# Kernel optimization log

Measured on AMD Instinct MI355X. Metric: run time of the kernel, lower is better.

## Reference

```python
import jax, jax.numpy as jnp
import numpy as np

N = 50000
E = 1600000
D_IN = 64
D_H = 64
D_EMB = 64
D_DEC = 128
B = 4096


def setup_inputs() -> dict:
    key = jax.random.key(0)
    ks = jax.random.split(key, 16)
    def lin(k, fan_in, fan_out):
        return jax.random.normal(k, (fan_in, fan_out), jnp.float32) / np.sqrt(fan_in)
    inp = {
        "x": jax.random.normal(ks[0], (N, D_IN), jnp.float32),
        "edge_index": jax.random.randint(ks[1], (2, E), 0, N),
        "drug_index": jax.random.randint(ks[2], (B, 2), 1, N),
        "bn_gamma": jnp.ones((D_IN,), jnp.float32),
        "bn_beta": jnp.zeros((D_IN,), jnp.float32),
        "Wu1": lin(ks[3], D_IN, D_H), "Wd1": lin(ks[4], D_IN, D_H), "Wb1": lin(ks[5], D_IN, D_H),
        "Wu2": lin(ks[6], 3 * D_H, D_H), "Wd2": lin(ks[7], 3 * D_H, D_H), "Wb2": lin(ks[8], 3 * D_H, D_H),
        "Wu3": lin(ks[9], 3 * D_H, D_EMB), "Wd3": lin(ks[10], 3 * D_H, D_EMB), "Wb3": lin(ks[11], 3 * D_H, D_EMB),
        "P1": jax.random.normal(ks[12], (3 * D_EMB, D_DEC), jnp.float32),
        "P2": jax.random.normal(ks[13], (D_DEC, D_DEC), jnp.float32),
    }
    return inp


def _batchnorm(x, gamma, beta, eps=1e-5):
    mu = jnp.mean(x, axis=0)
    var = jnp.var(x, axis=0)  # biased, matches torch BN training normalization
    return gamma * (x - mu) / jnp.sqrt(var + eps) + beta


def _bgnn_conv(x, row, col, Wu, Wd, Wb, n_nodes):
    # up direction: messages flow row -> col (source_to_target)
    up = x @ Wu
    dn = x @ Wd
    bi = x @ Wb
    ones = jnp.ones(row.shape[0], x.dtype)
    deg_up = jax.ops.segment_sum(ones, col, num_segments=n_nodes)  # in-degree at col
    x_up = jax.ops.segment_sum(up[row] / deg_up[col][:, None], col, num_segments=n_nodes)
    # down direction: flipped edge_index -> messages flow col -> row
    deg_dn = jax.ops.segment_sum(ones, row, num_segments=n_nodes)
    x_dn = jax.ops.segment_sum(dn[col] / deg_dn[row][:, None], row, num_segments=n_nodes)
    c = jnp.concatenate([x_up, x_dn, bi], axis=-1)
    nrm = jnp.linalg.norm(c, axis=-1, keepdims=True)
    return c / jnp.maximum(nrm, 1e-12)


def _leaky(t):
    return jnp.where(t >= 0, t, 0.1 * t)


def reference(x, edge_index, drug_index, bn_gamma, bn_beta,
              Wu1, Wd1, Wb1, Wu2, Wd2, Wb2, Wu3, Wd3, Wb3, P1, P2):
    row, col = edge_index[0], edge_index[1]
    h = _batchnorm(x, bn_gamma, bn_beta)
    h = _leaky(_bgnn_conv(h, row, col, Wu1, Wd1, Wb1, N))
    h = _leaky(_bgnn_conv(h, row, col, Wu2, Wd2, Wb2, N))
    h = _leaky(_bgnn_conv(h, row, col, Wu3, Wd3, Wb3, N))
    di = jnp.reshape(drug_index, (-1, 2))
    a = h[di[:, 0] - 1]  # [B, 3*D_EMB]
    b = h[di[:, 1] - 1]
    M = P1 @ P2 @ P1.T  # [3*D_EMB, 3*D_EMB]
    ypred = jnp.einsum('bd,de,be->b', a, M, b)[:, None]
    return ypred
```

## Files before the change

kernel.cpp:

```cpp
#include <hip/hip_runtime.h>

#define PN 50000
#define PE 1600000
#define PB 4096
#define NP 8
#define PSZ 6250
#define NSW 4
#define SWSZ 12500
#define SCAP 210000
#define NSL 4
#define GBLK 2048
#define NPER 7

typedef __attribute__((ext_vector_type(8))) short bf16x8;
typedef __attribute__((ext_vector_type(4))) float f32x4;

__device__ inline float b2f(ushort u) {
    union { unsigned int i; float f; } x; x.i = ((unsigned int)u) << 16; return x.f;
}
__device__ inline ushort f2b(float f) {
    union { float f; unsigned int i; } x; x.f = f;
    unsigned int r = (x.i + 0x7FFFu + ((x.i >> 16) & 1u)) >> 16;
    return (ushort)r;
}

static constexpr size_t L4N = 4 * (size_t)PN;
static constexpr size_t IDXCAP3 = PE + 3 * L4N + 1024;
static constexpr size_t OFF_BN     = 0;
static constexpr size_t OFF_GCUR   = 256;
static constexpr size_t OFF_TMPM   = 272;
static constexpr size_t OFF_M      = OFF_TMPM + 192 * 128;
static constexpr size_t OFF_WOFFU  = OFF_M + 192 * 192;
static constexpr size_t OFF_WOFFD  = OFF_WOFFU + L4N + 4;
static constexpr size_t OFF_WDEGU  = OFF_WOFFD + L4N + 4;
static constexpr size_t OFF_WDEGD  = OFF_WDEGU + L4N;
static constexpr size_t OFF_PHISTU = OFF_WDEGD + L4N;
static constexpr size_t OFF_PHISTD = OFF_PHISTU + NSL * L4N;
static constexpr size_t OFF_IDXU   = OFF_PHISTD + NSL * L4N;
static constexpr size_t OFF_IDXD   = OFF_IDXU + (IDXCAP3 + 1) / 2;
static constexpr size_t OFF_STGU   = OFF_IDXD + (IDXCAP3 + 1) / 2;
static constexpr size_t OFF_STGD   = OFF_STGU + NP * (size_t)SCAP;
static constexpr size_t OFF_WB16   = OFF_STGD + NP * (size_t)SCAP;
static constexpr size_t OFF_HB     = OFF_WB16 + 43008;
static constexpr size_t OFF_PROJ   = OFF_HB + (size_t)PN * 96;

__global__ __launch_bounds__(256) void bn_stats_kernel(const float* __restrict__ x,
                                                       float* __restrict__ sums, int N) {
    __shared__ float ls[256], ls2[256];
    int col = threadIdx.x & 63;
    int rstart = blockIdx.x * 4 + (threadIdx.x >> 6);
    float s = 0.f, s2 = 0.f;
    for (int r = rstart; r < N; r += gridDim.x * 4) {
        float v = x[(size_t)r * 64 + col];
        s += v; s2 += v * v;
    }
    ls[threadIdx.x] = s; ls2[threadIdx.x] = s2;
    __syncthreads();
    if (threadIdx.x < 64) {
        s  = ls[threadIdx.x]  + ls[threadIdx.x + 64]  + ls[threadIdx.x + 128]  + ls[threadIdx.x + 192];
        s2 = ls2[threadIdx.x] + ls2[threadIdx.x + 64] + ls2[threadIdx.x + 128] + ls2[threadIdx.x + 192];
        atomicAdd(&sums[col], s);
        atomicAdd(&sums[64 + col], s2);
    }
}

__global__ __launch_bounds__(64) void bn_finalize_kernel(const float* __restrict__ gamma,
                                                         const float* __restrict__ beta,
                                                         float* __restrict__ bn, int N) {
    int c = threadIdx.x;
    float mean = bn[c] / (float)N;
    float var = bn[64 + c] / (float)N - mean * mean;
    float sc = gamma[c] * rsqrtf(var + 1e-5f);
    bn[128 + c] = sc;
    bn[192 + c] = beta[c] - mean * sc;
}

__global__ __launch_bounds__(256) void bin_kernel(const int* __restrict__ ei,
                                                  int* __restrict__ gcur,
                                                  uint* __restrict__ stgu,
                                                  uint* __restrict__ stgd, int E) {
    __shared__ uint sbuf[16][1024];
    __shared__ int scnt[16], sbase[16];
    const int tid = threadIdx.x;
    for (int base = blockIdx.x * 1024; base < E; base += gridDim.x * 1024) {
        if (tid < 16) scnt[tid] = 0;
        __syncthreads();
#pragma unroll
        for (int j = 0; j < 4; ++j) {
            int e = base + j * 256 + tid;
            if (e < E) {
                int r = __builtin_nontemporal_load(&ei[e]);
                int c = __builtin_nontemporal_load(&ei[E + e]);
                int pu = c / PSZ;
                int slot = atomicAdd(&scnt[pu], 1);
                sbuf[pu][slot] = ((uint)c << 16) | (uint)r;
                int pd = r / PSZ;
                int slot2 = atomicAdd(&scnt[8 + pd], 1);
                sbuf[8 + pd][slot2] = ((uint)r << 16) | (uint)c;
            }
        }
        __syncthreads();
        if (tid < 16) sbase[tid] = atomicAdd(&gcur[tid], scnt[tid]);
        __syncthreads();
#pragma unroll 1
        for (int k = 0; k < 16; ++k) {
            int cnt = scnt[k];
            int gb = sbase[k];
            uint* dst = (k < 8) ? (stgu + (size_t)k * SCAP) : (stgd + (size_t)(k - 8) * SCAP);
            for (int i = tid; i < cnt; i += 256) {
                int gi = gb + i;
                if (gi < SCAP) dst[gi] = sbuf[k][i];
            }
        }
        __syncthreads();
    }
}

__global__ __launch_bounds__(256) void hist_kernel(const uint* __restrict__ stgu,
                                                   const uint* __restrict__ stgd,
                                                   const int* __restrict__ gcur,
                                                   int* __restrict__ phistu,
                                                   int* __restrict__ phistd) {
    __shared__ int hist[PSZ * NSW];
    const int p = blockIdx.x & 7;
    const int dir = (blockIdx.x >> 3) & 1;
    const int s = blockIdx.x >> 4;
    const int tid = threadIdx.x;
    const int lo = p * PSZ;
    for (int i = tid; i < PSZ * NSW; i += 256) hist[i] = 0;
    __syncthreads();
    const int cnt = min(gcur[dir * 8 + p], SCAP);
    const uint* stg = (dir ? stgd : stgu) + (size_t)p * SCAP;
    const int per = (cnt + NSL - 1) / NSL;
    const int s0 = s * per, s1 = min(cnt, s0 + per);
    for (int i = s0 + tid; i < s1; i += 256) {
        uint u = stg[i];
        int ld = (int)(u >> 16) - lo;
        int w = (int)(u & 0xFFFFu) / SWSZ;
        atomicAdd(&hist[ld * NSW + w], 1);
    }
    __syncthreads();
    int* ph = (dir ? phistd : phistu) + (size_t)s * L4N + (size_t)lo * NSW;
    for (int i = tid; i < PSZ * NSW; i += 256) ph[i] = hist[i];
}

__global__ __launch_bounds__(1024) void scan_kernel(const int* __restrict__ phA,
                                                    const int* __restrict__ phB,
                                                    int* __restrict__ offA,
                                                    int* __restrict__ offB,
                                                    int* __restrict__ degA,
                                                    int* __restrict__ degB, int len) {
    const int* ph = blockIdx.x ? phB : phA;
    int* off = blockIdx.x ? offB : offA;
    int* dego = blockIdx.x ? degB : degA;
    __shared__ int wsum[17];
    int tid = threadIdx.x, lane = tid & 63, wid = tid >> 6;
    int run = 0;
    for (int base = 0; base < len; base += 4096) {
        int i4 = base + tid * 4;
        int4 v = make_int4(0, 0, 0, 0);
        if (i4 < len) {
#pragma unroll
            for (int sl = 0; sl < NSL; ++sl) {
                int4 t = *(const int4*)&ph[(size_t)sl * len + i4];
                v.x += t.x; v.y += t.y; v.z += t.z; v.w += t.w;
            }
            *(int4*)&dego[i4] = v;
        }
        v.x = (v.x + 3) & ~3; v.y = (v.y + 3) & ~3;
        v.z = (v.z + 3) & ~3; v.w = (v.w + 3) & ~3;
        int lsum = v.x + v.y + v.z + v.w;
        int inc = lsum;
#pragma unroll
        for (int d = 1; d < 64; d <<= 1) {
            int t = __shfl_up(inc, d);
            if (lane >= d) inc += t;
        }
        if (lane == 63) wsum[wid] = inc;
        __syncthreads();
        if (tid == 0) {
            int r2 = 0;
#pragma unroll
            for (int i = 0; i < 16; ++i) { int t = wsum[i]; wsum[i] = r2; r2 += t; }
            wsum[16] = r2;
        }
        __syncthreads();
        if (i4 < len) {
            int pre = run + wsum[wid] + inc - lsum;
            int4 o;
            o.x = pre; o.y = pre + v.x; o.z = o.y + v.y; o.w = o.z + v.z;
            *(int4*)&off[i4] = o;
        }
        run += wsum[16];
        __syncthreads();
    }
    if (tid == 0) off[len] = run;
}

__global__ __launch_bounds__(256) void scatter_kernel(const uint* __restrict__ stgu,
                                                      const uint* __restrict__ stgd,
                                                      const int* __restrict__ gcur,
                                                      const int* __restrict__ phistu,
                                                      const int* __restrict__ phistd,
                                                      const int* __restrict__ woffu,
                                                      const int* __restrict__ woffd,
                                                      ushort* __restrict__ idxu,
                                                      ushort* __restrict__ idxd) {
    __shared__ int cur[PSZ * NSW];
    const int p = blockIdx.x & 7;
    const int dir = (blockIdx.x >> 3) & 1;
    const int s = blockIdx.x >> 4;
    const int tid = threadIdx.x;
    const int lo = p * PSZ;
    const int* off = (dir ? woffd : woffu);
    const int* phist = (dir ? phistd : phistu);
    const size_t gb = (size_t)lo * NSW;
    for (int i = tid; i < PSZ * NSW; i += 256) {
        int c = off[gb + i];
        for (int t = 0; t < s; ++t) c += phist[(size_t)t * L4N + gb + i];
        cur[i] = c;
    }
    __syncthreads();
    const int cnt = min(gcur[dir * 8 + p], SCAP);
    const uint* stg = (dir ? stgd : stgu) + (size_t)p * SCAP;
    ushort* idx = (dir ? idxd : idxu);
    const int per = (cnt + NSL - 1) / NSL;
    const int s0 = s * per, s1 = min(cnt, s0 + per);
    for (int i = s0 + tid; i < s1; i += 256) {
        uint u = stg[i];
        int src = (int)(u & 0xFFFFu);
        int li = ((int)(u >> 16) - lo) * NSW + src / SWSZ;
        int pos = atomicAdd(&cur[li], 1);
        idx[pos] = (ushort)src;
    }
}

template<int K>
__global__ __launch_bounds__(256) void wconv_kernel(const float* __restrict__ Wu,
                                                    const float* __restrict__ Wd,
                                                    const float* __restrict__ Wb,
                                                    ushort* __restrict__ out) {
    int idx = blockIdx.x * 256 + threadIdx.x;
    if (idx >= 192 * K) return;
    int c = idx / K, k = idx - c * K;
    const float* W = (c < 64) ? Wu : (c < 128 ? Wd : Wb);
    out[idx] = f2b(W[k * 64 + (c & 63)]);
}

template<int K, bool BN>
__global__ __launch_bounds__(256) void gemm_kernel(const ushort* __restrict__ hb,
                                                   const float* __restrict__ x,
                                                   const float* __restrict__ bn,
                                                   const ushort* __restrict__ wb,
                                                   ushort* __restrict__ proj, int nrows) {
    constexpr int KP = K + 8;
    __shared__ ushort wlds[192 * KP];
    const int tid = threadIdx.x;
    constexpr int KB8 = K / 8;
    for (int idx = tid; idx < 192 * KB8; idx += 256) {
        int col = idx / KB8, kb = idx - col * KB8;
        *(bf16x8*)&wlds[col * KP + kb * 8] = *(const bf16x8*)&wb[(size_t)col * K + kb * 8];
    }
    __syncthreads();
    const int lane = tid & 63, wid = tid >> 6;
    const int kgrp = (lane >> 4) * 8;
    const int rbase = blockIdx.x * 128 + wid * 32;
    int ar[2] = { min(rbase + (lane & 15), nrows - 1),
                  min(rbase + 16 + (lane & 15), nrows - 1) };
    f32x4 acc[2][12];
#pragma unroll
    for (int rt = 0; rt < 2; ++rt)
#pragma unroll
        for (int ct = 0; ct < 12; ++ct) acc[rt][ct] = (f32x4)0.0f;

#pragma unroll
    for (int k0 = 0; k0 < K; k0 += 32) {
        bf16x8 af[2];
        if (BN) {
#pragma unroll
            for (int rt = 0; rt < 2; ++rt)
#pragma unroll
                for (int j = 0; j < 8; ++j) {
                    int c = k0 + kgrp + j;
                    float v = x[(size_t)ar[rt] * 64 + c] * bn[128 + c] + bn[192 + c];
                    af[rt][j] = (short)f2b(v);
                }
        } else {
#pragma unroll
            for (int rt = 0; rt < 2; ++rt)
                af[rt] = *(const bf16x8*)&hb[(size_t)ar[rt] * 192 + k0 + kgrp];
        }
#pragma unroll
        for (int ct = 0; ct < 12; ++ct) {
            bf16x8 bfr = *(const bf16x8*)&wlds[(ct * 16 + (lane & 15)) * KP + k0 + kgrp];
            acc[0][ct] = __builtin_amdgcn_mfma_f32_16x16x32_bf16(af[0], bfr, acc[0][ct], 0, 0, 0);
            acc[1][ct] = __builtin_amdgcn_mfma_f32_16x16x32_bf16(af[1], bfr, acc[1][ct], 0, 0, 0);
        }
    }
    const int orow0 = blockIdx.x * 128 + wid * 32 + (lane >> 4) * 4;
#pragma unroll
    for (int rt = 0; rt < 2; ++rt)
#pragma unroll
        for (int ct = 0; ct < 12; ++ct) {
            int ocol = ct * 16 + (lane & 15);
#pragma unroll
            for (int j = 0; j < 4; ++j) {
                int orow = orow0 + rt * 16 + j;
                if (orow < nrows) proj[(size_t)orow * 192 + ocol] = f2b(acc[rt][ct][j]);
            }
        }
}

__global__ __launch_bounds__(256) void gather_kernel(const ushort* __restrict__ proj,
                                                     const int* __restrict__ woffu,
                                                     const int* __restrict__ wdegu,
                                                     const int* __restrict__ woffd,
                                                     const int* __restrict__ wdegd,
                                                     const ushort* __restrict__ idxu,
                                                     const ushort* __restrict__ idxd,
                                                     ushort* __restrict__ hb, int N) {
    const int gw = blockIdx.x * 4 + (threadIdx.x >> 6);
    const int nwaves = gridDim.x * 4;
    const int lane = threadIdx.x & 63;
    const int half = lane >> 5;
    const int sl = lane & 31;
    const int* __restrict__ woff = half ? woffd : woffu;
    const int* __restrict__ wdeg = half ? wdegd : wdegu;
    const ushort* __restrict__ idx = half ? idxd : idxu;
    const uint* __restrict__ rowb = (const uint*)proj + half * 32 + sl;

    float a0[NPER], a1[NPER];
    int dtot[NPER];
#pragma unroll
    for (int j = 0; j < NPER; ++j) { a0[j] = 0.f; a1[j] = 0.f; dtot[j] = 0; }

    for (int w = 0; w < NSW; ++w) {
#pragma unroll
        for (int j = 0; j < NPER; ++j) {
            int n = gw + j * nwaves;
            if (n < N) {
                int key = n * NSW + w;
                int s = woff[key];
                int cnt = wdeg[key];
                dtot[j] += cnt;
                const ushort* p = idx + s;
                for (int i = 0; i < cnt; i += 4) {
                    ushort4 U = *(const ushort4*)(p + i);
                    int v1 = (i + 1 < cnt), v2 = (i + 2 < cnt), v3 = (i + 3 < cnt);
                    int s0 = (int)U.x;
                    int s1 = v1 ? (int)U.y : 0;
                    int s2 = v2 ? (int)U.z : 0;
                    int s3 = v3 ? (int)U.w : 0;
                    uint w0 = rowb[(size_t)s0 * 96];
                    uint w1 = rowb[(size_t)s1 * 96];
                    uint w2 = rowb[(size_t)s2 * 96];
                    uint w3 = rowb[(size_t)s3 * 96];
                    if (!v1) w1 = 0; if (!v2) w2 = 0; if (!v3) w3 = 0;
                    a0[j] += __uint_as_float(w0 << 16) + __uint_as_float(w1 << 16)
                           + __uint_as_float(w2 << 16) + __uint_as_float(w3 << 16);
                    a1[j] += __uint_as_float(w0 & 0xFFFF0000u) + __uint_as_float(w1 & 0xFFFF0000u)
                           + __uint_as_float(w2 & 0xFFFF0000u) + __uint_as_float(w3 & 0xFFFF0000u);
                }
            }
        }
        __syncthreads();
    }

    uint* hb32 = (uint*)hb;
#pragma unroll
    for (int j = 0; j < NPER; ++j) {
        int n = gw + j * nwaves;
        if (n >= N) continue;
        float sc = 1.0f / (float)max(dtot[j], 1);
        float A0 = a0[j] * sc, A1 = a1[j] * sc;
        uint bw = (half == 0) ? ((const uint*)proj)[(size_t)n * 96 + 64 + sl] : 0u;
        float b0 = __uint_as_float(bw << 16);
        float b1 = __uint_as_float(bw & 0xFFFF0000u);
        float ss = A0 * A0 + A1 * A1 + b0 * b0 + b1 * b1;
#pragma unroll
        for (int off = 32; off; off >>= 1) ss += __shfl_xor(ss, off);
        float r = 1.0f / fmaxf(sqrtf(ss), 1e-12f);
        A0 *= r; A1 *= r; b0 *= r; b1 *= r;
        A0 = A0 >= 0.f ? A0 : 0.1f * A0;
        A1 = A1 >= 0.f ? A1 : 0.1f * A1;
        hb32[(size_t)n * 96 + half * 32 + sl] = (uint)f2b(A0) | ((uint)f2b(A1) << 16);
        if (half == 0) {
            b0 = b0 >= 0.f ? b0 : 0.1f * b0;
            b1 = b1 >= 0.f ? b1 : 0.1f * b1;
            hb32[(size_t)n * 96 + 64 + sl] = (uint)f2b(b0) | ((uint)f2b(b1) << 16);
        }
    }
}

__global__ __launch_bounds__(128) void m1_kernel(const float* __restrict__ P1,
                                                 const float* __restrict__ P2,
                                                 float* __restrict__ tmpM) {
    int i = blockIdx.x, c = threadIdx.x;
    float s = 0.f;
    for (int k = 0; k < 128; ++k) s += P1[i * 128 + k] * P2[k * 128 + c];
    tmpM[i * 128 + c] = s;
}

__global__ __launch_bounds__(192) void m2_kernel(const float* __restrict__ tmpM,
                                                 const float* __restrict__ P1,
                                                 float* __restrict__ M) {
    __shared__ float trow[128];
    int i = blockIdx.x, j = threadIdx.x;
    if (j < 128) trow[j] = tmpM[i * 128 + j];
    __syncthreads();
    float s = 0.f;
    for (int k = 0; k < 128; ++k) s += trow[k] * P1[j * 128 + k];
    M[i * 192 + j] = s;
}

__global__ __launch_bounds__(192) void decode_kernel(const ushort* __restrict__ hb,
                                                     const int* __restrict__ di,
                                                     const float* __restrict__ M,
                                                     float* __restrict__ out) {
    __shared__ alignas(16) float bvs[8][192];
    __shared__ float red[3][8];
    int pb = blockIdx.x * 8;
    int i = threadIdx.x;
#pragma unroll
    for (int p = 0; p < 8; ++p) {
        int nb = di[(pb + p) * 2 + 1] - 1;
        bvs[p][i] = b2f(hb[(size_t)nb * 192 + i]);
    }
    __syncthreads();
    float t[8] = {};
    const float4* M4 = (const float4*)(M + (size_t)i * 192);
    for (int j4 = 0; j4 < 48; ++j4) {
        float4 m = M4[j4];
#pragma unroll
        for (int p = 0; p < 8; ++p) {
            float4 b = *(const float4*)&bvs[p][j4 * 4];
            t[p] += m.x * b.x + m.y * b.y + m.z * b.z + m.w * b.w;
        }
    }
    int wid = i >> 6, lane = i & 63;
#pragma unroll
    for (int p = 0; p < 8; ++p) {
        int na = di[(pb + p) * 2] - 1;
        float v = b2f(hb[(size_t)na * 192 + i]) * t[p];
#pragma unroll
        for (int off = 32; off; off >>= 1) v += __shfl_xor(v, off);
        if (lane == 0) red[wid][p] = v;
    }
    __syncthreads();
    if (i < 8) out[pb + i] = red[0][i] + red[1][i] + red[2][i];
}

extern "C" void kernel_launch(void* const* d_in, const int* in_sizes, int n_in,
                              void* d_out, int out_size, void* d_ws, size_t ws_size,
                              hipStream_t stream) {
    const float* x     = (const float*)d_in[0];
    const int*   ei    = (const int*)d_in[1];
    const int*   di    = (const int*)d_in[2];
    const float* gamma = (const float*)d_in[3];
    const float* beta  = (const float*)d_in[4];
    const float* Wu[3] = {(const float*)d_in[5], (const float*)d_in[8],  (const float*)d_in[11]};
    const float* Wd[3] = {(const float*)d_in[6], (const float*)d_in[9],  (const float*)d_in[12]};
    const float* Wb[3] = {(const float*)d_in[7], (const float*)d_in[10], (const float*)d_in[13]};
    const float* P1    = (const float*)d_in[14];
    const float* P2    = (const float*)d_in[15];
    float* out = (float*)d_out;
    float* ws  = (float*)d_ws;

    float* bn    = ws + OFF_BN;
    int* gcur  = (int*)(ws + OFF_GCUR);
    float* tmpM  = ws + OFF_TMPM;
    float* M     = ws + OFF_M;
    int* woffu = (int*)(ws + OFF_WOFFU);
    int* woffd = (int*)(ws + OFF_WOFFD);
    int* wdegu = (int*)(ws + OFF_WDEGU);
    int* wdegd = (int*)(ws + OFF_WDEGD);
    int* phistu = (int*)(ws + OFF_PHISTU);
    int* phistd = (int*)(ws + OFF_PHISTD);
    ushort* idxu = (ushort*)(ws + OFF_IDXU);
    ushort* idxd = (ushort*)(ws + OFF_IDXD);
    uint* stgu = (uint*)(ws + OFF_STGU);
    uint* stgd = (uint*)(ws + OFF_STGD);
    ushort* wb16 = (ushort*)(ws + OFF_WB16);
    ushort* hb   = (ushort*)(ws + OFF_HB);
    ushort* proj = (ushort*)(ws + OFF_PROJ);
    ushort* wbl[3] = {wb16, wb16 + 12288, wb16 + 49152};

    hipMemsetAsync(ws, 0, 272 * sizeof(float), stream);

    bn_stats_kernel<<<200, 256, 0, stream>>>(x, bn, PN);
    bn_finalize_kernel<<<1, 64, 0, stream>>>(gamma, beta, bn, PN);

    bin_kernel<<<512, 256, 0, stream>>>(ei, gcur, stgu, stgd, PE);
    hist_kernel<<<16 * NSL, 256, 0, stream>>>(stgu, stgd, gcur, phistu, phistd);
    scan_kernel<<<2, 1024, 0, stream>>>(phistu, phistd, woffu, woffd, wdegu, wdegd, (int)L4N);
    scatter_kernel<<<16 * NSL, 256, 0, stream>>>(stgu, stgd, gcur, phistu, phistd,
                                                 woffu, woffd, idxu, idxd);

    wconv_kernel<64><<<(192 * 64 + 255) / 256, 256, 0, stream>>>(Wu[0], Wd[0], Wb[0], wbl[0]);
    wconv_kernel<192><<<(192 * 192 + 255) / 256, 256, 0, stream>>>(Wu[1], Wd[1], Wb[1], wbl[1]);
    wconv_kernel<192><<<(192 * 192 + 255) / 256, 256, 0, stream>>>(Wu[2], Wd[2], Wb[2], wbl[2]);

    const int ngb = (PN + 127) / 128;
    gemm_kernel<64, true><<<ngb, 256, 0, stream>>>(hb, x, bn, wbl[0], proj, PN);
    gather_kernel<<<GBLK, 256, 0, stream>>>(proj, woffu, wdegu, woffd, wdegd, idxu, idxd, hb, PN);
    gemm_kernel<192, false><<<ngb, 256, 0, stream>>>(hb, x, bn, wbl[1], proj, PN);
    gather_kernel<<<GBLK, 256, 0, stream>>>(proj, woffu, wdegu, woffd, wdegd, idxu, idxd, hb, PN);
    gemm_kernel<192, false><<<ngb, 256, 0, stream>>>(hb, x, bn, wbl[2], proj, PN);
    gather_kernel<<<GBLK, 256, 0, stream>>>(proj, woffu, wdegu, woffd, wdegd, idxu, idxd, hb, PN);

    m1_kernel<<<192, 128, 0, stream>>>(P1, P2, tmpM);
    m2_kernel<<<192, 192, 0, stream>>>(tmpM, P1, M);
    decode_kernel<<<PB / 8, 192, 0, stream>>>(hb, di, M, out);
}
```

Measured before the change: 752.3 us.

## Split hist/scatter by destination sub-range instead of edge slices

Hist and scatter blocks now each own a 625-node destination sub-range and scan the whole partition's staged edges, filtering by range. Previously blocks split the edge list into slices and wrote per-slice histograms that had to be summed in the scan and prefix-summed in scatter. This removes the per-slice histogram buffers, the extra scan reads and the scatter prefix loop. It also shrinks LDS per block and raises block count from 64 to 160. The cost is that each staged edge is read 10 times instead of once.

```diff
diff --git a/kernel.cpp b/kernel.cpp
--- a/kernel.cpp
+++ b/kernel.cpp
@@ -8,7 +8,8 @@
 #define NSW 4
 #define SWSZ 12500
 #define SCAP 210000
-#define NSL 4
+#define SP 10
+#define SPSZ 625
 #define GBLK 2048
 #define NPER 7
 
@@ -34,9 +35,7 @@
 static constexpr size_t OFF_WOFFD  = OFF_WOFFU + L4N + 4;
 static constexpr size_t OFF_WDEGU  = OFF_WOFFD + L4N + 4;
 static constexpr size_t OFF_WDEGD  = OFF_WDEGU + L4N;
-static constexpr size_t OFF_PHISTU = OFF_WDEGD + L4N;
-static constexpr size_t OFF_PHISTD = OFF_PHISTU + NSL * L4N;
-static constexpr size_t OFF_IDXU   = OFF_PHISTD + NSL * L4N;
+static constexpr size_t OFF_IDXU   = OFF_WDEGD + L4N;
 static constexpr size_t OFF_IDXD   = OFF_IDXU + (IDXCAP3 + 1) / 2;
 static constexpr size_t OFF_STGU   = OFF_IDXD + (IDXCAP3 + 1) / 2;
 static constexpr size_t OFF_STGD   = OFF_STGU + NP * (size_t)SCAP;
@@ -119,54 +118,42 @@
 __global__ __launch_bounds__(256) void hist_kernel(const uint* __restrict__ stgu,
                                                    const uint* __restrict__ stgd,
                                                    const int* __restrict__ gcur,
-                                                   int* __restrict__ phistu,
-                                                   int* __restrict__ phistd) {
-    __shared__ int hist[PSZ * NSW];
+                                                   int* __restrict__ wdegu,
+                                                   int* __restrict__ wdegd) {
+    __shared__ int hist[SPSZ * NSW];
     const int p = blockIdx.x & 7;
     const int dir = (blockIdx.x >> 3) & 1;
-    const int s = blockIdx.x >> 4;
+    const int sp = blockIdx.x >> 4;
     const int tid = threadIdx.x;
-    const int lo = p * PSZ;
-    for (int i = tid; i < PSZ * NSW; i += 256) hist[i] = 0;
+    const int lo = p * PSZ + sp * SPSZ;
+    for (int i = tid; i < SPSZ * NSW; i += 256) hist[i] = 0;
     __syncthreads();
     const int cnt = min(gcur[dir * 8 + p], SCAP);
     const uint* stg = (dir ? stgd : stgu) + (size_t)p * SCAP;
-    const int per = (cnt + NSL - 1) / NSL;
-    const int s0 = s * per, s1 = min(cnt, s0 + per);
-    for (int i = s0 + tid; i < s1; i += 256) {
+    for (int i = tid; i < cnt; i += 256) {
         uint u = stg[i];
         int ld = (int)(u >> 16) - lo;
-        int w = (int)(u & 0xFFFFu) / SWSZ;
-        atomicAdd(&hist[ld * NSW + w], 1);
-    }
-    __syncthreads();
-    int* ph = (dir ? phistd : phistu) + (size_t)s * L4N + (size_t)lo * NSW;
-    for (int i = tid; i < PSZ * NSW; i += 256) ph[i] = hist[i];
-}
-
-__global__ __launch_bounds__(1024) void scan_kernel(const int* __restrict__ phA,
-                                                    const int* __restrict__ phB,
+        if ((unsigned)ld < SPSZ)
+            atomicAdd(&hist[ld * NSW + (int)(u & 0xFFFFu) / SWSZ], 1);
+    }
+    __syncthreads();
+    int* wd = (dir ? wdegd : wdegu) + (size_t)lo * NSW;
+    for (int i = tid; i < SPSZ * NSW; i += 256) wd[i] = hist[i];
+}
+
+__global__ __launch_bounds__(1024) void scan_kernel(const int* __restrict__ degA,
+                                                    const int* __restrict__ degB,
                                                     int* __restrict__ offA,
-                                                    int* __restrict__ offB,
-                                                    int* __restrict__ degA,
-                                                    int* __restrict__ degB, int len) {
-    const int* ph = blockIdx.x ? phB : phA;
+                                                    int* __restrict__ offB, int len) {
+    const int* deg = blockIdx.x ? degB : degA;
     int* off = blockIdx.x ? offB : offA;
-    int* dego = blockIdx.x ? degB : degA;
     __shared__ int wsum[17];
     int tid = threadIdx.x, lane = tid & 63, wid = tid >> 6;
     int run = 0;
     for (int base = 0; base < len; base += 4096) {
         int i4 = base + tid * 4;
         int4 v = make_int4(0, 0, 0, 0);
-        if (i4 < len) {
-#pragma unroll
-            for (int sl = 0; sl < NSL; ++sl) {
-                int4 t = *(const int4*)&ph[(size_t)sl * len + i4];
-                v.x += t.x; v.y += t.y; v.z += t.z; v.w += t.w;
-            }
-            *(int4*)&dego[i4] = v;
-        }
+        if (i4 < len) v = *(const int4*)&deg[i4];
         v.x = (v.x + 3) & ~3; v.y = (v.y + 3) & ~3;
         v.z = (v.z + 3) & ~3; v.w = (v.w + 3) & ~3;
         int lsum = v.x + v.y + v.z + v.w;
@@ -200,38 +187,30 @@
 __global__ __launch_bounds__(256) void scatter_kernel(const uint* __restrict__ stgu,
                                                       const uint* __restrict__ stgd,
                                                       const int* __restrict__ gcur,
-                                                      const int* __restrict__ phistu,
-                                                      const int* __restrict__ phistd,
                                                       const int* __restrict__ woffu,
                                                       const int* __restrict__ woffd,
                                                       ushort* __restrict__ idxu,
                                                       ushort* __restrict__ idxd) {
-    __shared__ int cur[PSZ * NSW];
+    __shared__ int cur[SPSZ * NSW];
     const int p = blockIdx.x & 7;
     const int dir = (blockIdx.x >> 3) & 1;
-    const int s = blockIdx.x >> 4;
+    const int sp = blockIdx.x >> 4;
     const int tid = threadIdx.x;
-    const int lo = p * PSZ;
-    const int* off = (dir ? woffd : woffu);
-    const int* phist = (dir ? phistd : phistu);
-    const size_t gb = (size_t)lo * NSW;
-    for (int i = tid; i < PSZ * NSW; i += 256) {
-        int c = off[gb + i];
-        for (int t = 0; t < s; ++t) c += phist[(size_t)t * L4N + gb + i];
-        cur[i] = c;
-    }
+    const int lo = p * PSZ + sp * SPSZ;
+    const int* woff = (dir ? woffd : woffu) + (size_t)lo * NSW;
+    for (int i = tid; i < SPSZ * NSW; i += 256) cur[i] = woff[i];
     __syncthreads();
     const int cnt = min(gcur[dir * 8 + p], SCAP);
     const uint* stg = (dir ? stgd : stgu) + (size_t)p * SCAP;
     ushort* idx = (dir ? idxd : idxu);
-    const int per = (cnt + NSL - 1) / NSL;
-    const int s0 = s * per, s1 = min(cnt, s0 + per);
-    for (int i = s0 + tid; i < s1; i += 256) {
+    for (int i = tid; i < cnt; i += 256) {
         uint u = stg[i];
-        int src = (int)(u & 0xFFFFu);
-        int li = ((int)(u >> 16) - lo) * NSW + src / SWSZ;
-        int pos = atomicAdd(&cur[li], 1);
-        idx[pos] = (ushort)src;
+        int ld = (int)(u >> 16) - lo;
+        if ((unsigned)ld < SPSZ) {
+            int src = (int)(u & 0xFFFFu);
+            int pos = atomicAdd(&cur[ld * NSW + src / SWSZ], 1);
+            idx[pos] = (ushort)src;
+        }
     }
 }
 
@@ -474,8 +453,6 @@
     int* woffd = (int*)(ws + OFF_WOFFD);
     int* wdegu = (int*)(ws + OFF_WDEGU);
     int* wdegd = (int*)(ws + OFF_WDEGD);
-    int* phistu = (int*)(ws + OFF_PHISTU);
-    int* phistd = (int*)(ws + OFF_PHISTD);
     ushort* idxu = (ushort*)(ws + OFF_IDXU);
     ushort* idxd = (ushort*)(ws + OFF_IDXD);
     uint* stgu = (uint*)(ws + OFF_STGU);
@@ -491,10 +468,9 @@
     bn_finalize_kernel<<<1, 64, 0, stream>>>(gamma, beta, bn, PN);
 
     bin_kernel<<<512, 256, 0, stream>>>(ei, gcur, stgu, stgd, PE);
-    hist_kernel<<<16 * NSL, 256, 0, stream>>>(stgu, stgd, gcur, phistu, phistd);
-    scan_kernel<<<2, 1024, 0, stream>>>(phistu, phistd, woffu, woffd, wdegu, wdegd, (int)L4N);
-    scatter_kernel<<<16 * NSL, 256, 0, stream>>>(stgu, stgd, gcur, phistu, phistd,
-                                                 woffu, woffd, idxu, idxd);
+    hist_kernel<<<NP * 2 * SP, 256, 0, stream>>>(stgu, stgd, gcur, wdegu, wdegd);
+    scan_kernel<<<2, 1024, 0, stream>>>(wdegu, wdegd, woffu, woffd, (int)L4N);
+    scatter_kernel<<<NP * 2 * SP, 256, 0, stream>>>(stgu, stgd, gcur, woffu, woffd, idxu, idxd);
 
     wconv_kernel<64><<<(192 * 64 + 255) / 256, 256, 0, stream>>>(Wu[0], Wd[0], Wb[0], wbl[0]);
     wconv_kernel<192><<<(192 * 192 + 255) / 256, 256, 0, stream>>>(Wu[1], Wd[1], Wb[1], wbl[1]);
```

Measured after the change: 921.1 us. 22.4% more time.

## Add rebin pass splitting edge partitions by source window for wider hist/scatter

Applied to the files above, without the earlier changes.

Adds a rebin kernel that splits each destination partition's staged edges into four chunks by source window. This lets the histogram and scatter kernels run 256 blocks instead of 64, each with a smaller 6250-entry shared array. The aim is more parallelism and occupancy in the CSR build. In exchange it adds an extra read/write pass over all edges and a fixed per-chunk capacity (CCAP) that could overflow on skewed inputs.

```diff
diff --git a/kernel.cpp b/kernel.cpp
--- a/kernel.cpp
+++ b/kernel.cpp
@@ -8,7 +8,8 @@
 #define NSW 4
 #define SWSZ 12500
 #define SCAP 210000
-#define NSL 4
+#define CCAP 60000
+#define NSL2 4
 #define GBLK 2048
 #define NPER 7
 
@@ -28,19 +29,21 @@
 static constexpr size_t IDXCAP3 = PE + 3 * L4N + 1024;
 static constexpr size_t OFF_BN     = 0;
 static constexpr size_t OFF_GCUR   = 256;
-static constexpr size_t OFF_TMPM   = 272;
+static constexpr size_t OFF_CCUR   = 272;
+static constexpr size_t OFF_TMPM   = 336;
 static constexpr size_t OFF_M      = OFF_TMPM + 192 * 128;
 static constexpr size_t OFF_WOFFU  = OFF_M + 192 * 192;
 static constexpr size_t OFF_WOFFD  = OFF_WOFFU + L4N + 4;
 static constexpr size_t OFF_WDEGU  = OFF_WOFFD + L4N + 4;
 static constexpr size_t OFF_WDEGD  = OFF_WDEGU + L4N;
 static constexpr size_t OFF_PHISTU = OFF_WDEGD + L4N;
-static constexpr size_t OFF_PHISTD = OFF_PHISTU + NSL * L4N;
-static constexpr size_t OFF_IDXU   = OFF_PHISTD + NSL * L4N;
+static constexpr size_t OFF_PHISTD = OFF_PHISTU + NSL2 * L4N;
+static constexpr size_t OFF_IDXU   = OFF_PHISTD + NSL2 * L4N;
 static constexpr size_t OFF_IDXD   = OFF_IDXU + (IDXCAP3 + 1) / 2;
 static constexpr size_t OFF_STGU   = OFF_IDXD + (IDXCAP3 + 1) / 2;
 static constexpr size_t OFF_STGD   = OFF_STGU + NP * (size_t)SCAP;
-static constexpr size_t OFF_WB16   = OFF_STGD + NP * (size_t)SCAP;
+static constexpr size_t OFF_CHK    = OFF_STGD + NP * (size_t)SCAP;
+static constexpr size_t OFF_WB16   = OFF_CHK + 64 * (size_t)CCAP;
 static constexpr size_t OFF_HB     = OFF_WB16 + 43008;
 static constexpr size_t OFF_PROJ   = OFF_HB + (size_t)PN * 96;
 
@@ -116,32 +119,75 @@
     }
 }
 
-__global__ __launch_bounds__(256) void hist_kernel(const uint* __restrict__ stgu,
-                                                   const uint* __restrict__ stgd,
-                                                   const int* __restrict__ gcur,
+__global__ __launch_bounds__(256) void rebin_kernel(const uint* __restrict__ stgu,
+                                                    const uint* __restrict__ stgd,
+                                                    const int* __restrict__ gcur,
+                                                    int* __restrict__ ccur,
+                                                    uint* __restrict__ chk) {
+    __shared__ uint sb[4][1024];
+    __shared__ int sc[4], sbase[4];
+    const int p = blockIdx.x & 7;
+    const int dir = (blockIdx.x >> 3) & 1;
+    const int sl = blockIdx.x >> 4;
+    const int tid = threadIdx.x;
+    const int cnt = min(gcur[dir * 8 + p], SCAP);
+    const uint* stg = (dir ? stgd : stgu) + (size_t)p * SCAP;
+    const int cbase = p + dir * 8;
+    const int per = (cnt + 7) / 8;
+    const int s0 = sl * per, s1 = min(cnt, s0 + per);
+    for (int base = s0; base < s1; base += 1024) {
+        if (tid < 4) sc[tid] = 0;
+        __syncthreads();
+#pragma unroll
+        for (int j = 0; j < 4; ++j) {
+            int i = base + j * 256 + tid;
+            if (i < s1) {
+                uint u = stg[i];
+                int w = (int)(u & 0xFFFFu) / SWSZ;
+                int slot = atomicAdd(&sc[w], 1);
+                sb[w][slot] = u;
+            }
+        }
+        __syncthreads();
+        if (tid < 4) sbase[tid] = atomicAdd(&ccur[cbase + 16 * tid], sc[tid]);
+        __syncthreads();
+#pragma unroll 1
+        for (int k = 0; k < 4; ++k) {
+            int ck = sc[k];
+            int gb = sbase[k];
+            uint* dst = chk + (size_t)(cbase + 16 * k) * CCAP;
+            for (int i = tid; i < ck; i += 256) {
+                int gi = gb + i;
+                if (gi < CCAP) dst[gi] = sb[k][i];
+            }
+        }
+        __syncthreads();
+    }
+}
+
+__global__ __launch_bounds__(256) void hist_kernel(const uint* __restrict__ chk,
+                                                   const int* __restrict__ ccur,
                                                    int* __restrict__ phistu,
                                                    int* __restrict__ phistd) {
-    __shared__ int hist[PSZ * NSW];
-    const int p = blockIdx.x & 7;
-    const int dir = (blockIdx.x >> 3) & 1;
-    const int s = blockIdx.x >> 4;
+    __shared__ int hist[PSZ];
+    const int c = blockIdx.x & 63;
+    const int s = blockIdx.x >> 6;
+    const int p = c & 7;
+    const int dir = (c >> 3) & 1;
+    const int w = c >> 4;
     const int tid = threadIdx.x;
     const int lo = p * PSZ;
-    for (int i = tid; i < PSZ * NSW; i += 256) hist[i] = 0;
-    __syncthreads();
-    const int cnt = min(gcur[dir * 8 + p], SCAP);
-    const uint* stg = (dir ? stgd : stgu) + (size_t)p * SCAP;
-    const int per = (cnt + NSL - 1) / NSL;
+    for (int i = tid; i < PSZ; i += 256) hist[i] = 0;
+    __syncthreads();
+    const int cnt = min(ccur[c], CCAP);
+    const uint* stg = chk + (size_t)c * CCAP;
+    const int per = (cnt + NSL2 - 1) / NSL2;
     const int s0 = s * per, s1 = min(cnt, s0 + per);
-    for (int i = s0 + tid; i < s1; i += 256) {
-        uint u = stg[i];
-        int ld = (int)(u >> 16) - lo;
-        int w = (int)(u & 0xFFFFu) / SWSZ;
-        atomicAdd(&hist[ld * NSW + w], 1);
-    }
-    __syncthreads();
-    int* ph = (dir ? phistd : phistu) + (size_t)s * L4N + (size_t)lo * NSW;
-    for (int i = tid; i < PSZ * NSW; i += 256) ph[i] = hist[i];
+    for (int i = s0 + tid; i < s1; i += 256)
+        atomicAdd(&hist[(int)(stg[i] >> 16) - lo], 1);
+    __syncthreads();
+    int* ph = (dir ? phistd : phistu) + (size_t)s * L4N;
+    for (int i = tid; i < PSZ; i += 256) ph[(size_t)(lo + i) * NSW + w] = hist[i];
 }
 
 __global__ __launch_bounds__(1024) void scan_kernel(const int* __restrict__ phA,
@@ -161,7 +207,7 @@
         int4 v = make_int4(0, 0, 0, 0);
         if (i4 < len) {
 #pragma unroll
-            for (int sl = 0; sl < NSL; ++sl) {
+            for (int sl = 0; sl < NSL2; ++sl) {
                 int4 t = *(const int4*)&ph[(size_t)sl * len + i4];
                 v.x += t.x; v.y += t.y; v.z += t.z; v.w += t.w;
             }
@@ -197,41 +243,40 @@
     if (tid == 0) off[len] = run;
 }
 
-__global__ __launch_bounds__(256) void scatter_kernel(const uint* __restrict__ stgu,
-                                                      const uint* __restrict__ stgd,
-                                                      const int* __restrict__ gcur,
+__global__ __launch_bounds__(256) void scatter_kernel(const uint* __restrict__ chk,
+                                                      const int* __restrict__ ccur,
                                                       const int* __restrict__ phistu,
                                                       const int* __restrict__ phistd,
                                                       const int* __restrict__ woffu,
                                                       const int* __restrict__ woffd,
                                                       ushort* __restrict__ idxu,
                                                       ushort* __restrict__ idxd) {
-    __shared__ int cur[PSZ * NSW];
-    const int p = blockIdx.x & 7;
-    const int dir = (blockIdx.x >> 3) & 1;
-    const int s = blockIdx.x >> 4;
+    __shared__ int cur[PSZ];
+    const int c = blockIdx.x & 63;
+    const int s = blockIdx.x >> 6;
+    const int p = c & 7;
+    const int dir = (c >> 3) & 1;
+    const int w = c >> 4;
     const int tid = threadIdx.x;
     const int lo = p * PSZ;
-    const int* off = (dir ? woffd : woffu);
+    const int* woff = (dir ? woffd : woffu);
     const int* phist = (dir ? phistd : phistu);
-    const size_t gb = (size_t)lo * NSW;
-    for (int i = tid; i < PSZ * NSW; i += 256) {
-        int c = off[gb + i];
-        for (int t = 0; t < s; ++t) c += phist[(size_t)t * L4N + gb + i];
-        cur[i] = c;
-    }
-    __syncthreads();
-    const int cnt = min(gcur[dir * 8 + p], SCAP);
-    const uint* stg = (dir ? stgd : stgu) + (size_t)p * SCAP;
+    for (int i = tid; i < PSZ; i += 256) {
+        size_t key = (size_t)(lo + i) * NSW + w;
+        int cv = woff[key];
+        for (int t = 0; t < s; ++t) cv += phist[(size_t)t * L4N + key];
+        cur[i] = cv;
+    }
+    __syncthreads();
+    const int cnt = min(ccur[c], CCAP);
+    const uint* stg = chk + (size_t)c * CCAP;
     ushort* idx = (dir ? idxd : idxu);
-    const int per = (cnt + NSL - 1) / NSL;
+    const int per = (cnt + NSL2 - 1) / NSL2;
     const int s0 = s * per, s1 = min(cnt, s0 + per);
     for (int i = s0 + tid; i < s1; i += 256) {
         uint u = stg[i];
-        int src = (int)(u & 0xFFFFu);
-        int li = ((int)(u >> 16) - lo) * NSW + src / SWSZ;
-        int pos = atomicAdd(&cur[li], 1);
-        idx[pos] = (ushort)src;
+        int pos = atomicAdd(&cur[(int)(u >> 16) - lo], 1);
+        idx[pos] = (ushort)(u & 0xFFFFu);
     }
 }
 
@@ -468,6 +513,7 @@
 
     float* bn    = ws + OFF_BN;
     int* gcur  = (int*)(ws + OFF_GCUR);
+    int* ccur  = (int*)(ws + OFF_CCUR);
     float* tmpM  = ws + OFF_TMPM;
     float* M     = ws + OFF_M;
     int* woffu = (int*)(ws + OFF_WOFFU);
@@ -480,21 +526,23 @@
     ushort* idxd = (ushort*)(ws + OFF_IDXD);
     uint* stgu = (uint*)(ws + OFF_STGU);
     uint* stgd = (uint*)(ws + OFF_STGD);
+    uint* chk  = (uint*)(ws + OFF_CHK);
     ushort* wb16 = (ushort*)(ws + OFF_WB16);
     ushort* hb   = (ushort*)(ws + OFF_HB);
     ushort* proj = (ushort*)(ws + OFF_PROJ);
     ushort* wbl[3] = {wb16, wb16 + 12288, wb16 + 49152};
 
-    hipMemsetAsync(ws, 0, 272 * sizeof(float), stream);
+    hipMemsetAsync(ws, 0, 336 * sizeof(float), stream);
 
     bn_stats_kernel<<<200, 256, 0, stream>>>(x, bn, PN);
     bn_finalize_kernel<<<1, 64, 0, stream>>>(gamma, beta, bn, PN);
 
     bin_kernel<<<512, 256, 0, stream>>>(ei, gcur, stgu, stgd, PE);
-    hist_kernel<<<16 * NSL, 256, 0, stream>>>(stgu, stgd, gcur, phistu, phistd);
+    rebin_kernel<<<128, 256, 0, stream>>>(stgu, stgd, gcur, ccur, chk);
+    hist_kernel<<<64 * NSL2, 256, 0, stream>>>(chk, ccur, phistu, phistd);
     scan_kernel<<<2, 1024, 0, stream>>>(phistu, phistd, woffu, woffd, wdegu, wdegd, (int)L4N);
-    scatter_kernel<<<16 * NSL, 256, 0, stream>>>(stgu, stgd, gcur, phistu, phistd,
-                                                 woffu, woffd, idxu, idxd);
+    scatter_kernel<<<64 * NSL2, 256, 0, stream>>>(chk, ccur, phistu, phistd,
+                                                  woffu, woffd, idxu, idxd);
 
     wconv_kernel<64><<<(192 * 64 + 255) / 256, 256, 0, stream>>>(Wu[0], Wd[0], Wb[0], wbl[0]);
     wconv_kernel<192><<<(192 * 192 + 255) / 256, 256, 0, stream>>>(Wu[1], Wd[1], Wb[1], wbl[1]);
```

After: 699.5 us. 1.08x faster.
